# Optimization experiments

Measured on AMD Instinct MI355X. Metric: run time of the kernel, lower is better.

The kernel has to match this reference:

```python
import jax, jax.numpy as jnp
import numpy as np

C = 256
G = 32            # GroupNorm groups = min(32, C)
DQK = C // 8      # q/k channel dim
EPS = 1e-5


def setup_inputs() -> dict:
    key = jax.random.key(0)
    ks = jax.random.split(key, 10)
    B, H, W = 4, 64, 64
    s = 0.02
    return {
        "x": jax.random.normal(ks[0], (B, C, H, W), dtype=jnp.float32),
        "gamma": jnp.ones((C,), jnp.float32),
        "beta": jnp.zeros((C,), jnp.float32),
        "wq": jax.random.normal(ks[1], (DQK, C), jnp.float32) * s,
        "bq": jnp.zeros((DQK,), jnp.float32),
        "wk": jax.random.normal(ks[2], (DQK, C), jnp.float32) * s,
        "bk": jnp.zeros((DQK,), jnp.float32),
        "wv": jax.random.normal(ks[3], (C, C), jnp.float32) * s,
        "bv": jnp.zeros((C,), jnp.float32),
        "wp": jax.random.normal(ks[4], (C, C), jnp.float32) * s,
        "bp": jnpp if False else jnp.zeros((C,), jnp.float32),
    }


def reference(x, gamma, beta, wq, bq, wk, bk, wv, bv, wp, bp):
    B, Cc, H, W = x.shape
    N = H * W
    # GroupNorm(32, C), affine
    h = x.reshape(B, G, Cc // G, H, W)
    mu = h.mean(axis=(2, 3, 4), keepdims=True)
    var = h.var(axis=(2, 3, 4), keepdims=True)
    h = (h - mu) * jax.lax.rsqrt(var + EPS)
    h = h.reshape(B, Cc, N) * gamma[:, None] + beta[:, None]
    # 1x1 convs == per-token linear maps over channels
    q = jnp.einsum('dc,bcn->bnd', wq, h) + bq            # [B, N, DQK]
    k = jnp.einsum('dc,bcn->bdn', wk, h) + bk[:, None]   # [B, DQK, N]
    v = jnp.einsum('ec,bcn->ben', wv, h) + bv[:, None]   # [B, C, N]
    scale = DQK ** (-0.5)
    attn = jax.nn.softmax(jnp.einsum('bnd,bdm->bnm', q, k) * scale, axis=-1)
    out = jnp.einsum('bnm,bem->ben', attn, v)            # [B, C, N]
    proj = jnp.einsum('fe,ben->bfn', wp, out) + bp[:, None]
    return x + proj.reshape(B, Cc, H, W)
```

## Files before the change

kernel.cpp:

```cpp
#include <hip/hip_runtime.h>
#include <hip/hip_bf16.h>

#define NB 4
#define CD 256
#define NT 4096
#define DQ 32

typedef __attribute__((ext_vector_type(8))) __bf16 bf16x8;
typedef __attribute__((ext_vector_type(4))) float float4v;
typedef __attribute__((ext_vector_type(16))) float float16v;
typedef __attribute__((ext_vector_type(4))) unsigned int uint4v;
typedef __attribute__((ext_vector_type(2))) unsigned int uint2v;

#if __has_builtin(__builtin_amdgcn_exp2f)
#define EXP2(x) __builtin_amdgcn_exp2f(x)
#else
#define EXP2(x) exp2f(x)
#endif

__device__ inline unsigned short f2bf(float f) {
  unsigned u = __float_as_uint(f);
  u += 0x7fffu + ((u >> 16) & 1u);
  return (unsigned short)(u >> 16);
}

__global__ __launch_bounds__(256) void gn_stats(
    const float* __restrict__ x, float* __restrict__ accum) {
  int bg = blockIdx.x >> 2, ch = blockIdx.x & 3;
  int tid = threadIdx.x;
  const float4* xp = (const float4*)(x + (size_t)bg * 32768 + ch * 8192);
  float s = 0.f, ss = 0.f;
#pragma unroll
  for (int i = 0; i < 8; i++) {
    float4 v = xp[tid + 256 * i];
    s += v.x + v.y + v.z + v.w;
    ss += v.x * v.x + v.y * v.y + v.z * v.z + v.w * v.w;
  }
  int wid = tid >> 6, lane = tid & 63;
#pragma unroll
  for (int off = 32; off >= 1; off >>= 1) {
    s += __shfl_xor(s, off);
    ss += __shfl_xor(ss, off);
  }
  __shared__ float red[8];
  if (lane == 0) { red[wid] = s; red[4 + wid] = ss; }
  __syncthreads();
  if (tid == 0) {
    atomicAdd(&accum[2 * bg], red[0] + red[1] + red[2] + red[3]);
    atomicAdd(&accum[2 * bg + 1], red[4] + red[5] + red[6] + red[7]);
  }
}

__global__ __launch_bounds__(256) void gn_apply(
    const float* __restrict__ x, const float* __restrict__ gamma,
    const float* __restrict__ beta, const float* __restrict__ accum,
    unsigned short* __restrict__ h) {
  int bg = blockIdx.x >> 2, nc = blockIdx.x & 3;
  int tid = threadIdx.x;
  float mu = accum[2 * bg] * (1.f / 32768.f);
  float var = accum[2 * bg + 1] * (1.f / 32768.f) - mu * mu;
  float rstd = rsqrtf(var + 1e-5f);
  int b = bg >> 5, g = bg & 31, c0 = g * 8;
  float gam[8], bet[8];
#pragma unroll
  for (int j = 0; j < 8; j++) { gam[j] = gamma[c0 + j]; bet[j] = beta[c0 + j]; }
  const float* xb = x + (size_t)bg * 32768;
#pragma unroll
  for (int i = 0; i < 4; i++) {
    int n = nc * 1024 + tid + 256 * i;
    unsigned short hv[8];
#pragma unroll
    for (int j = 0; j < 8; j++) {
      float y = (xb[j * NT + n] - mu) * rstd * gam[j] + bet[j];
      hv[j] = f2bf(y);
    }
    *(uint4v*)(h + ((size_t)(b * NT + n) * CD + c0)) = *(uint4v*)hv;
  }
}

__global__ __launch_bounds__(256) void conv_w(
    const float* __restrict__ wq, const float* __restrict__ wk,
    const float* __restrict__ wv, const float* __restrict__ wp,
    const float* __restrict__ bq, const float* __restrict__ bk,
    const float* __restrict__ bv, unsigned short* __restrict__ wqkv,
    unsigned short* __restrict__ wpb, float* __restrict__ bias) {
  const float scale2 = 0.2550348909867343f;
  int i = blockIdx.x * 256 + threadIdx.x;
  if (i < 320 * 256) {
    int j = i >> 8, c = i & 255;
    float v;
    if (j < 32) v = wq[j * 256 + c] * scale2;
    else if (j < 64) v = wk[(j - 32) * 256 + c];
    else v = wv[(j - 64) * 256 + c];
    wqkv[i] = f2bf(v);
  } else if (i < 320 * 256 + 256 * 256) {
    int k = i - 320 * 256;
    wpb[k] = f2bf(wp[k]);
  } else if (i < 320 * 256 + 256 * 256 + 320) {
    int j = i - (320 * 256 + 256 * 256);
    float v;
    if (j < 32) v = bq[j] * scale2;
    else if (j < 64) v = bk[j - 32];
    else v = bv[j - 64];
    bias[j] = v;
  }
}

__global__ __launch_bounds__(256) void qkv_gemm(
    const unsigned short* __restrict__ A, const unsigned short* __restrict__ H,
    const float* __restrict__ bias, unsigned short* __restrict__ qk,
    unsigned short* __restrict__ v) {
  int nt = blockIdx.x, mt = blockIdx.y, b = blockIdx.z;
  int tid = threadIdx.x, lane = tid & 63;
  int w = tid >> 6, mi = w & 1, ni = w >> 1;
  int l31 = lane & 31, hh = lane >> 5;
  int m_base = mt * 64 + 32 * mi;
  int n_base = nt * 128 + 64 * ni;
  const unsigned short* Arow = A + (size_t)(m_base + l31) * 256 + 8 * hh;
  const unsigned short* Hb = H + (size_t)b * NT * CD;
  const unsigned short* h0 = Hb + (size_t)(n_base + l31) * CD + 8 * hh;
  const unsigned short* h1 = h0 + (size_t)32 * CD;
  float16v acc0, acc1;
#pragma unroll
  for (int r = 0; r < 16; r++) { acc0[r] = 0.f; acc1[r] = 0.f; }
#pragma unroll
  for (int s = 0; s < 16; s++) {
    bf16x8 af = *(const bf16x8*)(Arow + 16 * s);
    bf16x8 b0 = *(const bf16x8*)(h0 + 16 * s);
    bf16x8 b1 = *(const bf16x8*)(h1 + 16 * s);
    acc0 = __builtin_amdgcn_mfma_f32_32x32x16_bf16(af, b0, acc0, 0, 0, 0);
    acc1 = __builtin_amdgcn_mfma_f32_32x32x16_bf16(af, b1, acc1, 0, 0, 0);
  }
  float bj[16];
  int jr[16];
#pragma unroll
  for (int r = 0; r < 16; r++) {
    jr[r] = m_base + (r & 3) + 8 * (r >> 2) + 4 * hh;
    bj[r] = bias[jr[r]];
  }
#pragma unroll
  for (int half = 0; half < 2; half++) {
    int n = n_base + 32 * half + l31;
#pragma unroll
    for (int r = 0; r < 16; r++) {
      float val = (half ? acc1[r] : acc0[r]) + bj[r];
      int j = jr[r];
      if (j < 64) {
        qk[((size_t)b * NT + n) * 64 + j] = f2bf(val);
      } else {
        v[((size_t)b * CD + (j - 64)) * NT + n] = f2bf(val);
      }
    }
  }
}

__global__ __launch_bounds__(256) void attn_fused(
    const unsigned short* __restrict__ qk, const unsigned short* __restrict__ V,
    unsigned short* __restrict__ O) {
  int n0 = blockIdx.x * 64;
  int E0 = blockIdx.y * 128;
  int b = blockIdx.z;
  int tid = threadIdx.x, lane = tid & 63, w = tid >> 6;
  int qi = w & 1, ei = w >> 1;
  int l31 = lane & 31, hh = lane >> 5;

  __shared__ unsigned short Ks[64 * 36];
  __shared__ unsigned short Vs[128 * 68];
  __shared__ unsigned short Pb[2 * 32 * 68];
  __shared__ float lsp[2][2][32];

  const unsigned short* qkb = qk + (size_t)b * NT * 64;
  const unsigned short* Vb = V + (size_t)b * CD * NT;

  int n_g = n0 + 32 * qi + l31;
  bf16x8 qfr[2];
  qfr[0] = *(const bf16x8*)&qkb[(size_t)n_g * 64 + 8 * hh];
  qfr[1] = *(const bf16x8*)&qkb[(size_t)n_g * 64 + 8 * hh + 16];

  int se = tid >> 1, smh = (tid & 1) * 32;
  int skr = tid >> 2, skc = (tid & 3) * 8;

  uint4v vreg[4];
  uint4v kreg;
  {
    const unsigned short* vp = &Vb[(size_t)(E0 + se) * NT + smh];
#pragma unroll
    for (int u = 0; u < 4; u++) vreg[u] = *(const uint4v*)(vp + 8 * u);
    kreg = *(const uint4v*)&qkb[(size_t)skr * 64 + 32 + skc];
  }

  float16v acc[2];
#pragma unroll
  for (int et = 0; et < 2; et++)
#pragma unroll
    for (int r = 0; r < 16; r++) acc[et][r] = 0.f;
  float lsum = 0.f;
  unsigned short* Prow = &Pb[(qi * 32 + l31) * 68];

  for (int it = 0; it < 64; it++) {
    *(uint4v*)&Ks[skr * 36 + skc] = kreg;
    if (it + 1 < 64) {
      int m1 = (it + 1) * 64;
      kreg = *(const uint4v*)&qkb[(size_t)(m1 + skr) * 64 + 32 + skc];
    }
    __syncthreads();

#pragma unroll
    for (int u = 0; u < 4; u++)
      *(uint4v*)&Vs[se * 68 + smh + 8 * u] = vreg[u];
    if (it + 1 < 64) {
      int m1 = (it + 1) * 64;
      const unsigned short* vp = &Vb[(size_t)(E0 + se) * NT + m1 + smh];
#pragma unroll
      for (int u = 0; u < 4; u++) vreg[u] = *(const uint4v*)(vp + 8 * u);
    }

    float16v st;
#pragma unroll
    for (int r = 0; r < 16; r++) st[r] = 0.f;
#pragma unroll
    for (int s = 0; s < 2; s++) {
      bf16x8 af = *(const bf16x8*)&Ks[(32 * ei + l31) * 36 + 16 * s + 8 * hh];
      st = __builtin_amdgcn_mfma_f32_32x32x16_bf16(af, qfr[s], st, 0, 0, 0);
    }
#pragma unroll
    for (int rq = 0; rq < 4; rq++) {
      float e0 = EXP2(st[4 * rq + 0]);
      float e1 = EXP2(st[4 * rq + 1]);
      float e2 = EXP2(st[4 * rq + 2]);
      float e3 = EXP2(st[4 * rq + 3]);
      lsum += (e0 + e1) + (e2 + e3);
      uint2v pw;
      pw[0] = __builtin_amdgcn_perm(__float_as_uint(e1), __float_as_uint(e0),
                                    0x07060302u);
      pw[1] = __builtin_amdgcn_perm(__float_as_uint(e3), __float_as_uint(e2),
                                    0x07060302u);
      *(uint2v*)&Prow[8 * rq + 4 * hh + 32 * ei] = pw;
    }
    __syncthreads();

#pragma unroll
    for (int sp = 0; sp < 4; sp++) {
      bf16x8 afr = *(const bf16x8*)&Pb[(qi * 32 + l31) * 68 + 16 * sp + 8 * hh];
#pragma unroll
      for (int et = 0; et < 2; et++) {
        bf16x8 bfr = *(const bf16x8*)&Vs[(64 * ei + 32 * et + l31) * 68 +
                                         16 * sp + 8 * hh];
        acc[et] =
            __builtin_amdgcn_mfma_f32_32x32x16_bf16(afr, bfr, acc[et], 0, 0, 0);
      }
    }
  }

  lsum += __shfl_xor(lsum, 32);
  if (hh == 0) lsp[qi][ei][l31] = lsum;
  __syncthreads();
  unsigned short* Ob = O + (size_t)b * NT * CD;
#pragma unroll
  for (int r = 0; r < 16; r++) {
    int nl = (r & 3) + 8 * (r >> 2) + 4 * hh;
    float l = lsp[qi][0][nl] + lsp[qi][1][nl];
    float inv = 1.f / l;
    size_t row = (size_t)(n0 + 32 * qi + nl) * CD + E0 + 64 * ei + l31;
#pragma unroll
    for (int et = 0; et < 2; et++) {
      Ob[row + 32 * et] = f2bf(acc[et][r] * inv);
    }
  }
}

__global__ __launch_bounds__(256) void proj_gemm(
    const unsigned short* __restrict__ Wp, const unsigned short* __restrict__ O,
    const float* __restrict__ bp, const float* __restrict__ x,
    float* __restrict__ out) {
  int nt = blockIdx.x, mt = blockIdx.y, b = blockIdx.z;
  int tid = threadIdx.x, lane = tid & 63;
  int w = tid >> 6, mi = w & 1, ni = w >> 1;
  int l31 = lane & 31, hh = lane >> 5;
  int m_base = mt * 64 + 32 * mi;
  int n_base = nt * 128 + 64 * ni;
  const unsigned short* Arow = Wp + (size_t)(m_base + l31) * 256 + 8 * hh;
  const unsigned short* Ob = O + (size_t)b * NT * CD;
  const unsigned short* o0 = Ob + (size_t)(n_base + l31) * CD + 8 * hh;
  const unsigned short* o1 = o0 + (size_t)32 * CD;
  float16v acc0, acc1;
#pragma unroll
  for (int r = 0; r < 16; r++) { acc0[r] = 0.f; acc1[r] = 0.f; }
#pragma unroll
  for (int s = 0; s < 16; s++) {
    bf16x8 af = *(const bf16x8*)(Arow + 16 * s);
    bf16x8 b0 = *(const bf16x8*)(o0 + 16 * s);
    bf16x8 b1 = *(const bf16x8*)(o1 + 16 * s);
    acc0 = __builtin_amdgcn_mfma_f32_32x32x16_bf16(af, b0, acc0, 0, 0, 0);
    acc1 = __builtin_amdgcn_mfma_f32_32x32x16_bf16(af, b1, acc1, 0, 0, 0);
  }
#pragma unroll
  for (int half = 0; half < 2; half++) {
    int n = n_base + 32 * half + l31;
#pragma unroll
    for (int r = 0; r < 16; r++) {
      int f = m_base + (r & 3) + 8 * (r >> 2) + 4 * hh;
      size_t idx = ((size_t)b * CD + f) * NT + n;
      out[idx] = x[idx] + (half ? acc1[r] : acc0[r]) + bp[f];
    }
  }
}

extern "C" void kernel_launch(void* const* d_in, const int* in_sizes, int n_in,
                              void* d_out, int out_size, void* d_ws,
                              size_t ws_size, hipStream_t stream) {
  (void)in_sizes; (void)n_in; (void)out_size; (void)ws_size;
  const float* x = (const float*)d_in[0];
  const float* gamma = (const float*)d_in[1];
  const float* beta = (const float*)d_in[2];
  const float* wq = (const float*)d_in[3];
  const float* bq = (const float*)d_in[4];
  const float* wk = (const float*)d_in[5];
  const float* bk = (const float*)d_in[6];
  const float* wv = (const float*)d_in[7];
  const float* bv = (const float*)d_in[8];
  const float* wp = (const float*)d_in[9];
  const float* bp = (const float*)d_in[10];
  float* out = (float*)d_out;

  char* ws = (char*)d_ws;
  unsigned short* h_ws = (unsigned short*)ws;
  unsigned short* qk_ws = (unsigned short*)(ws + 8388608);
  unsigned short* v_ws = (unsigned short*)(ws + 10485760);
  unsigned short* o_ws = (unsigned short*)(ws + 18874368);
  unsigned short* wqkv_b = (unsigned short*)(ws + 27262976);
  unsigned short* wp_b = (unsigned short*)(ws + 27426816);
  float* bias_q = (float*)(ws + 27557888);
  float* accum = (float*)(ws + 27559168);

  hipMemsetAsync(accum, 0, 1024, stream);
  gn_stats<<<512, 256, 0, stream>>>(x, accum);
  conv_w<<<578, 256, 0, stream>>>(wq, wk, wv, wp, bq, bk, bv, wqkv_b, wp_b,
                                  bias_q);
  gn_apply<<<512, 256, 0, stream>>>(x, gamma, beta, accum, h_ws);
  dim3 gq(32, 5, NB);
  qkv_gemm<<<gq, 256, 0, stream>>>(wqkv_b, h_ws, bias_q, qk_ws, v_ws);
  dim3 ga(64, 2, NB);
  attn_fused<<<ga, 256, 0, stream>>>(qk_ws, v_ws, o_ws);
  dim3 gp(32, 4, NB);
  proj_gemm<<<gp, 256, 0, stream>>>(wp_b, o_ws, bp, x, out);
}
```

Measured before the change: 208.7 us.

## Split attention over key halves and merge partial sums in projection GEMM

The attention kernel now splits the key/value sequence into two halves, doubling the grid. Each block writes unnormalized partial outputs and per-row exp-sums to workspace, with h_ws reused for one half. The projection GEMM adds the two partials, normalizes by the combined sums while loading its B fragments, then runs the MFMAs. Separately, the GroupNorm stats and weight conversion kernels are merged into one launch that writes per-chunk sums instead of using atomics, which drops the memset. Costs: extra partial-output traffic and an extra bf16 rounding of the unnormalized partials.

New measurement: 207.9 us. No clear change (-0.4%).

```diff
diff --git a/kernel.cpp b/kernel.cpp
--- a/kernel.cpp
+++ b/kernel.cpp
@@ -24,30 +24,59 @@
   return (unsigned short)(u >> 16);
 }
 
-__global__ __launch_bounds__(256) void gn_stats(
-    const float* __restrict__ x, float* __restrict__ accum) {
-  int bg = blockIdx.x >> 2, ch = blockIdx.x & 3;
+__global__ __launch_bounds__(256) void gn_prep(
+    const float* __restrict__ x, float* __restrict__ accum,
+    const float* __restrict__ wq, const float* __restrict__ wk,
+    const float* __restrict__ wv, const float* __restrict__ wp,
+    const float* __restrict__ bq, const float* __restrict__ bk,
+    const float* __restrict__ bv, unsigned short* __restrict__ wqkv,
+    unsigned short* __restrict__ wpb, float* __restrict__ bias) {
+  int bx = blockIdx.x;
   int tid = threadIdx.x;
-  const float4* xp = (const float4*)(x + (size_t)bg * 32768 + ch * 8192);
-  float s = 0.f, ss = 0.f;
-#pragma unroll
-  for (int i = 0; i < 8; i++) {
-    float4 v = xp[tid + 256 * i];
-    s += v.x + v.y + v.z + v.w;
-    ss += v.x * v.x + v.y * v.y + v.z * v.z + v.w * v.w;
-  }
-  int wid = tid >> 6, lane = tid & 63;
-#pragma unroll
-  for (int off = 32; off >= 1; off >>= 1) {
-    s += __shfl_xor(s, off);
-    ss += __shfl_xor(ss, off);
-  }
-  __shared__ float red[8];
-  if (lane == 0) { red[wid] = s; red[4 + wid] = ss; }
-  __syncthreads();
-  if (tid == 0) {
-    atomicAdd(&accum[2 * bg], red[0] + red[1] + red[2] + red[3]);
-    atomicAdd(&accum[2 * bg + 1], red[4] + red[5] + red[6] + red[7]);
+  if (bx < 512) {
+    int bg = bx >> 2, ch = bx & 3;
+    const float4* xp = (const float4*)(x + (size_t)bg * 32768 + ch * 8192);
+    float s = 0.f, ss = 0.f;
+#pragma unroll
+    for (int i = 0; i < 8; i++) {
+      float4 v = xp[tid + 256 * i];
+      s += v.x + v.y + v.z + v.w;
+      ss += v.x * v.x + v.y * v.y + v.z * v.z + v.w * v.w;
+    }
+    int wid = tid >> 6, lane = tid & 63;
+#pragma unroll
+    for (int off = 32; off >= 1; off >>= 1) {
+      s += __shfl_xor(s, off);
+      ss += __shfl_xor(ss, off);
+    }
+    __shared__ float red[8];
+    if (lane == 0) { red[wid] = s; red[4 + wid] = ss; }
+    __syncthreads();
+    if (tid == 0) {
+      accum[2 * bx] = red[0] + red[1] + red[2] + red[3];
+      accum[2 * bx + 1] = red[4] + red[5] + red[6] + red[7];
+    }
+  } else {
+    const float scale2 = 0.2550348909867343f;
+    int i = (bx - 512) * 256 + tid;
+    if (i < 320 * 256) {
+      int j = i >> 8, c = i & 255;
+      float v;
+      if (j < 32) v = wq[j * 256 + c] * scale2;
+      else if (j < 64) v = wk[(j - 32) * 256 + c];
+      else v = wv[(j - 64) * 256 + c];
+      wqkv[i] = f2bf(v);
+    } else if (i < 320 * 256 + 256 * 256) {
+      int k = i - 320 * 256;
+      wpb[k] = f2bf(wp[k]);
+    } else if (i < 320 * 256 + 256 * 256 + 320) {
+      int j = i - (320 * 256 + 256 * 256);
+      float v;
+      if (j < 32) v = bq[j] * scale2;
+      else if (j < 64) v = bk[j - 32];
+      else v = bv[j - 64];
+      bias[j] = v;
+    }
   }
 }
 
@@ -57,8 +86,12 @@
     unsigned short* __restrict__ h) {
   int bg = blockIdx.x >> 2, nc = blockIdx.x & 3;
   int tid = threadIdx.x;
-  float mu = accum[2 * bg] * (1.f / 32768.f);
-  float var = accum[2 * bg + 1] * (1.f / 32768.f) - mu * mu;
+  float S = accum[8 * bg] + accum[8 * bg + 2] + accum[8 * bg + 4] +
+            accum[8 * bg + 6];
+  float SS = accum[8 * bg + 1] + accum[8 * bg + 3] + accum[8 * bg + 5] +
+             accum[8 * bg + 7];
+  float mu = S * (1.f / 32768.f);
+  float var = SS * (1.f / 32768.f) - mu * mu;
   float rstd = rsqrtf(var + 1e-5f);
   int b = bg >> 5, g = bg & 31, c0 = g * 8;
   float gam[8], bet[8];
@@ -75,34 +108,6 @@
       hv[j] = f2bf(y);
     }
     *(uint4v*)(h + ((size_t)(b * NT + n) * CD + c0)) = *(uint4v*)hv;
-  }
-}
-
-__global__ __launch_bounds__(256) void conv_w(
-    const float* __restrict__ wq, const float* __restrict__ wk,
-    const float* __restrict__ wv, const float* __restrict__ wp,
-    const float* __restrict__ bq, const float* __restrict__ bk,
-    const float* __restrict__ bv, unsigned short* __restrict__ wqkv,
-    unsigned short* __restrict__ wpb, float* __restrict__ bias) {
-  const float scale2 = 0.2550348909867343f;
-  int i = blockIdx.x * 256 + threadIdx.x;
-  if (i < 320 * 256) {
-    int j = i >> 8, c = i & 255;
-    float v;
-    if (j < 32) v = wq[j * 256 + c] * scale2;
-    else if (j < 64) v = wk[(j - 32) * 256 + c];
-    else v = wv[(j - 64) * 256 + c];
-    wqkv[i] = f2bf(v);
-  } else if (i < 320 * 256 + 256 * 256) {
-    int k = i - 320 * 256;
-    wpb[k] = f2bf(wp[k]);
-  } else if (i < 320 * 256 + 256 * 256 + 320) {
-    int j = i - (320 * 256 + 256 * 256);
-    float v;
-    if (j < 32) v = bq[j] * scale2;
-    else if (j < 64) v = bk[j - 32];
-    else v = bv[j - 64];
-    bias[j] = v;
   }
 }
 
@@ -156,8 +161,11 @@
 
 __global__ __launch_bounds__(256) void attn_fused(
     const unsigned short* __restrict__ qk, const unsigned short* __restrict__ V,
-    unsigned short* __restrict__ O) {
-  int n0 = blockIdx.x * 64;
+    unsigned short* __restrict__ Pa, unsigned short* __restrict__ Pb,
+    float* __restrict__ lp4) {
+  int bx = blockIdx.x;
+  int n0 = (bx >> 1) * 64;
+  int kh = bx & 1;
   int E0 = blockIdx.y * 128;
   int b = blockIdx.z;
   int tid = threadIdx.x, lane = tid & 63, w = tid >> 6;
@@ -166,8 +174,7 @@
 
   __shared__ unsigned short Ks[64 * 36];
   __shared__ unsigned short Vs[128 * 68];
-  __shared__ unsigned short Pb[2 * 32 * 68];
-  __shared__ float lsp[2][2][32];
+  __shared__ unsigned short Pbuf[2 * 32 * 68];
 
   const unsigned short* qkb = qk + (size_t)b * NT * 64;
   const unsigned short* Vb = V + (size_t)b * CD * NT;
@@ -180,13 +187,14 @@
   int se = tid >> 1, smh = (tid & 1) * 32;
   int skr = tid >> 2, skc = (tid & 3) * 8;
 
+  int mbase = kh * 2048;
   uint4v vreg[4];
   uint4v kreg;
   {
-    const unsigned short* vp = &Vb[(size_t)(E0 + se) * NT + smh];
+    const unsigned short* vp = &Vb[(size_t)(E0 + se) * NT + mbase + smh];
 #pragma unroll
     for (int u = 0; u < 4; u++) vreg[u] = *(const uint4v*)(vp + 8 * u);
-    kreg = *(const uint4v*)&qkb[(size_t)skr * 64 + 32 + skc];
+    kreg = *(const uint4v*)&qkb[(size_t)(mbase + skr) * 64 + 32 + skc];
   }
 
   float16v acc[2];
@@ -195,12 +203,12 @@
 #pragma unroll
     for (int r = 0; r < 16; r++) acc[et][r] = 0.f;
   float lsum = 0.f;
-  unsigned short* Prow = &Pb[(qi * 32 + l31) * 68];
-
-  for (int it = 0; it < 64; it++) {
+  unsigned short* Prow = &Pbuf[(qi * 32 + l31) * 68];
+
+  for (int it = 0; it < 32; it++) {
     *(uint4v*)&Ks[skr * 36 + skc] = kreg;
-    if (it + 1 < 64) {
-      int m1 = (it + 1) * 64;
+    if (it + 1 < 32) {
+      int m1 = mbase + (it + 1) * 64;
       kreg = *(const uint4v*)&qkb[(size_t)(m1 + skr) * 64 + 32 + skc];
     }
     __syncthreads();
@@ -208,8 +216,8 @@
 #pragma unroll
     for (int u = 0; u < 4; u++)
       *(uint4v*)&Vs[se * 68 + smh + 8 * u] = vreg[u];
-    if (it + 1 < 64) {
-      int m1 = (it + 1) * 64;
+    if (it + 1 < 32) {
+      int m1 = mbase + (it + 1) * 64;
       const unsigned short* vp = &Vb[(size_t)(E0 + se) * NT + m1 + smh];
 #pragma unroll
       for (int u = 0; u < 4; u++) vreg[u] = *(const uint4v*)(vp + 8 * u);
@@ -241,7 +249,8 @@
 
 #pragma unroll
     for (int sp = 0; sp < 4; sp++) {
-      bf16x8 afr = *(const bf16x8*)&Pb[(qi * 32 + l31) * 68 + 16 * sp + 8 * hh];
+      bf16x8 afr =
+          *(const bf16x8*)&Pbuf[(qi * 32 + l31) * 68 + 16 * sp + 8 * hh];
 #pragma unroll
       for (int et = 0; et < 2; et++) {
         bf16x8 bfr = *(const bf16x8*)&Vs[(64 * ei + 32 * et + l31) * 68 +
@@ -253,24 +262,42 @@
   }
 
   lsum += __shfl_xor(lsum, 32);
-  if (hh == 0) lsp[qi][ei][l31] = lsum;
-  __syncthreads();
-  unsigned short* Ob = O + (size_t)b * NT * CD;
+  unsigned short* Pout = (kh ? Pb : Pa) + (size_t)b * NT * CD;
 #pragma unroll
   for (int r = 0; r < 16; r++) {
     int nl = (r & 3) + 8 * (r >> 2) + 4 * hh;
-    float l = lsp[qi][0][nl] + lsp[qi][1][nl];
-    float inv = 1.f / l;
     size_t row = (size_t)(n0 + 32 * qi + nl) * CD + E0 + 64 * ei + l31;
 #pragma unroll
     for (int et = 0; et < 2; et++) {
-      Ob[row + 32 * et] = f2bf(acc[et][r] * inv);
-    }
-  }
+      Pout[row + 32 * et] = f2bf(acc[et][r]);
+    }
+  }
+  if (hh == 0) {
+    lp4[(size_t)((kh * 2 + ei) * NB + b) * NT + n0 + 32 * qi + l31] = lsum;
+  }
+}
+
+__device__ inline bf16x8 combine_frag(const unsigned short* p0,
+                                      const unsigned short* p1, float inv) {
+  uint4v ua = *(const uint4v*)p0;
+  uint4v ub = *(const uint4v*)p1;
+  uint4v r;
+#pragma unroll
+  for (int j = 0; j < 4; j++) {
+    float lo = __uint_as_float(ua[j] << 16) + __uint_as_float(ub[j] << 16);
+    float hi = __uint_as_float(ua[j] & 0xffff0000u) +
+               __uint_as_float(ub[j] & 0xffff0000u);
+    lo *= inv;
+    hi *= inv;
+    r[j] = __builtin_amdgcn_perm(__float_as_uint(hi), __float_as_uint(lo),
+                                 0x07060302u);
+  }
+  return *(bf16x8*)&r;
 }
 
 __global__ __launch_bounds__(256) void proj_gemm(
-    const unsigned short* __restrict__ Wp, const unsigned short* __restrict__ O,
+    const unsigned short* __restrict__ Wp, const unsigned short* __restrict__ Pa,
+    const unsigned short* __restrict__ Pb, const float* __restrict__ lp4,
     const float* __restrict__ bp, const float* __restrict__ x,
     float* __restrict__ out) {
   int nt = blockIdx.x, mt = blockIdx.y, b = blockIdx.z;
@@ -280,17 +307,26 @@
   int m_base = mt * 64 + 32 * mi;
   int n_base = nt * 128 + 64 * ni;
   const unsigned short* Arow = Wp + (size_t)(m_base + l31) * 256 + 8 * hh;
-  const unsigned short* Ob = O + (size_t)b * NT * CD;
-  const unsigned short* o0 = Ob + (size_t)(n_base + l31) * CD + 8 * hh;
-  const unsigned short* o1 = o0 + (size_t)32 * CD;
+  int nA = n_base + l31, nB = nA + 32;
+  float lA = 0.f, lB = 0.f;
+#pragma unroll
+  for (int s4 = 0; s4 < 4; s4++) {
+    lA += lp4[(size_t)(s4 * NB + b) * NT + nA];
+    lB += lp4[(size_t)(s4 * NB + b) * NT + nB];
+  }
+  float invA = 1.f / lA, invB = 1.f / lB;
+  const unsigned short* a0 = Pa + ((size_t)b * NT + nA) * CD + 8 * hh;
+  const unsigned short* a1 = Pa + ((size_t)b * NT + nB) * CD + 8 * hh;
+  const unsigned short* c0 = Pb + ((size_t)b * NT + nA) * CD + 8 * hh;
+  const unsigned short* c1 = Pb + ((size_t)b * NT + nB) * CD + 8 * hh;
   float16v acc0, acc1;
 #pragma unroll
   for (int r = 0; r < 16; r++) { acc0[r] = 0.f; acc1[r] = 0.f; }
 #pragma unroll
   for (int s = 0; s < 16; s++) {
     bf16x8 af = *(const bf16x8*)(Arow + 16 * s);
-    bf16x8 b0 = *(const bf16x8*)(o0 + 16 * s);
-    bf16x8 b1 = *(const bf16x8*)(o1 + 16 * s);
+    bf16x8 b0 = combine_frag(a0 + 16 * s, c0 + 16 * s, invA);
+    bf16x8 b1 = combine_frag(a1 + 16 * s, c1 + 16 * s, invB);
     acc0 = __builtin_amdgcn_mfma_f32_32x32x16_bf16(af, b0, acc0, 0, 0, 0);
     acc1 = __builtin_amdgcn_mfma_f32_32x32x16_bf16(af, b1, acc1, 0, 0, 0);
   }
@@ -332,16 +368,15 @@
   unsigned short* wp_b = (unsigned short*)(ws + 27426816);
   float* bias_q = (float*)(ws + 27557888);
   float* accum = (float*)(ws + 27559168);
-
-  hipMemsetAsync(accum, 0, 1024, stream);
-  gn_stats<<<512, 256, 0, stream>>>(x, accum);
-  conv_w<<<578, 256, 0, stream>>>(wq, wk, wv, wp, bq, bk, bv, wqkv_b, wp_b,
-                                  bias_q);
+  float* lp4 = (float*)(ws + 27563264);
+
+  gn_prep<<<1090, 256, 0, stream>>>(x, accum, wq, wk, wv, wp, bq, bk, bv,
+                                    wqkv_b, wp_b, bias_q);
   gn_apply<<<512, 256, 0, stream>>>(x, gamma, beta, accum, h_ws);
   dim3 gq(32, 5, NB);
   qkv_gemm<<<gq, 256, 0, stream>>>(wqkv_b, h_ws, bias_q, qk_ws, v_ws);
-  dim3 ga(64, 2, NB);
-  attn_fused<<<ga, 256, 0, stream>>>(qk_ws, v_ws, o_ws);
+  dim3 ga(128, 2, NB);
+  attn_fused<<<ga, 256, 0, stream>>>(qk_ws, v_ws, h_ws, o_ws, lp4);
   dim3 gp(32, 4, NB);
-  proj_gemm<<<gp, 256, 0, stream>>>(wp_b, o_ws, bp, x, out);
-}
+  proj_gemm<<<gp, 256, 0, stream>>>(wp_b, h_ws, o_ws, lp4, bp, x, out);
+}
```
